# Performance work log

Hardware: AMD Instinct MI355X
Metric: run time of the kernel (lower is better)

## Reference

```python
import jax, jax.numpy as jnp
import numpy as np

N_NODES = 50000
N_EDGES = 800000
K_HOPS = 4
F_IN, F_HID, A_DIM = 6, 128, 3


def gcn_norm(edge_index, edge_weight, num_nodes):
    # TAGConv(normalize=True) uses gcn_norm WITHOUT added self-loops:
    # norm = D^{-1/2}[src] * w * D^{-1/2}[dst], deg computed at target (col).
    row, col = edge_index[0], edge_index[1]
    deg = jax.ops.segment_sum(edge_weight, col, num_segments=num_nodes)
    deg_inv_sqrt = jnp.where(deg > 0, jax.lax.rsqrt(deg), 0.0)
    return deg_inv_sqrt[row] * edge_weight * deg_inv_sqrt[col]


def tag_conv(x, edge_index, norm_w, W, b):
    # out = sum_{k=0..K} (A_hat^k x) @ W[k] + b ; W: [K+1, in, out]
    row, col = edge_index[0], edge_index[1]
    out = x @ W[0]
    xk = x
    for k in range(1, W.shape[0]):
        # one sparse propagation hop: gather at src, scale, scatter-add at dst
        xk = jax.ops.segment_sum(norm_w[:, None] * xk[row], col, num_segments=x.shape[0])
        out = out + xk @ W[k]
    return out + b


def setup_inputs() -> dict:
    key = jax.random.key(0)
    ks = jax.random.split(key, 5)
    x = jax.random.normal(ks[0], (N_NODES, F_IN), dtype=jnp.float32)
    edge_index = jax.random.randint(ks[1], (2, N_EDGES), 0, N_NODES, dtype=jnp.int32)
    edge_weight = jax.random.uniform(ks[2], (N_EDGES,), dtype=jnp.float32)
    s1 = float(1.0 / np.sqrt(F_IN))
    s2 = float(1.0 / np.sqrt(F_HID))
    W1 = jax.random.uniform(ks[3], (K_HOPS + 1, F_IN, F_HID), minval=-s1, maxval=s1, dtype=jnp.float32)
    b1 = jnp.zeros((F_HID,), jnp.float32)
    W2 = jax.random.uniform(ks[4], (K_HOPS + 1, F_HID, 2 * A_DIM), minval=-s2, maxval=s2, dtype=jnp.float32)
    b2 = jnp.zeros((2 * A_DIM,), jnp.float32)
    return {"x": x, "edge_index": edge_index, "edge_weight": edge_weight,
            "W1": W1, "b1": b1, "W2": W2, "b2": b2}


def reference(x, edge_index, edge_weight, W1, b1, W2, b2):
    norm_w = gcn_norm(edge_index, edge_weight, x.shape[0])
    h = jax.nn.relu(tag_conv(x, edge_index, norm_w, W1, b1))
    out = tag_conv(h, edge_index, norm_w, W2, b2)
    mu = jnp.tanh(out[..., :A_DIM])
    logvar = jnp.tanh(out[..., A_DIM:])
    sigma = jnp.exp(2.0 * logvar)
    return mu, sigma
```

## Files before the change

### kernel.cpp

```cpp
#include <hip/hip_runtime.h>

#define NN 50000
#define NE 800000
#define KH 4
#define FIN 6
#define FH 128
#define FO 6
#define ADIM 3
#define NN6 (NN * 6)
#define NN8 (NN * 8)
#define NBKT 196
#define EPB 2048
#define NPB 391
#define CAP 6144
#define ROWMASK 0xFFFFFu
#define NEPAD (NE + NBKT * 1024)

typedef unsigned int u32;
typedef _Float16 f16;
typedef f16 f16x8 __attribute__((ext_vector_type(8)));

struct __align__(8) Edge { u32 r; float w; };

__device__ __forceinline__ float h2f_bits(u32 hb) {
    union { unsigned short us; f16 h; } c; c.us = (unsigned short)hb; return (float)c.h;
}
__device__ __forceinline__ u32 f2h_bits(float f) {
    union { unsigned short us; f16 h; } c; c.h = (f16)f; return (u32)c.us;
}
__device__ __forceinline__ u32 pack2(float a, float b) {
    return f2h_bits(a) | (f2h_bits(b) << 16);
}

__global__ void bucket_hist(const int* __restrict__ col, u32* __restrict__ ghist) {
    __shared__ u32 h[NBKT];
    for (int t = threadIdx.x; t < NBKT; t += 256) h[t] = 0;
    __syncthreads();
    int base = blockIdx.x * EPB;
#pragma unroll
    for (int i = 0; i < EPB / 256; ++i) {
        int e = base + i * 256 + threadIdx.x;
        if (e < NE) atomicAdd(&h[((u32)col[e]) >> 8], 1u);
    }
    __syncthreads();
    for (int t = threadIdx.x; t < NBKT; t += 256)
        if (h[t]) atomicAdd(&ghist[t], h[t]);
}

__global__ void bucket_scan(const u32* __restrict__ ghist, u32* __restrict__ bbase,
                            u32* __restrict__ bcur,
                            const float* __restrict__ W1, const float* __restrict__ W2,
                            float* __restrict__ W1T, float* __restrict__ W2T) {
    __shared__ u32 sh[256];
    int t = threadIdx.x;
    u32 v = (t < NBKT) ? ghist[t] : 0;
    sh[t] = v;
    __syncthreads();
    for (int off = 1; off < 256; off <<= 1) {
        u32 u = (t >= off) ? sh[t - off] : 0;
        __syncthreads();
        sh[t] += u;
        __syncthreads();
    }
    if (t < NBKT) { bbase[t] = sh[t] - v; bcur[t] = sh[t] - v; }
    if (t == NBKT - 1) bbase[NBKT] = sh[t];
    for (int idx = t; idx < 30 * FH; idx += 256) {
        int f = idx / 30, i = idx - f * 30;
        W1T[idx] = W1[i * FH + f];
        int k = i / 6, a = i - k * 6;
        W2T[idx] = W2[((size_t)k * FH + f) * FO + a];
    }
}

__global__ __launch_bounds__(256) void partition_kernel(
        const int* __restrict__ row, const int* __restrict__ col,
        const float* __restrict__ w, u32* __restrict__ bcur,
        Edge* __restrict__ etmp) {
    __shared__ u32 hcnt[NBKT];
    __shared__ u32 hloc[NBKT];
    __shared__ u32 hglb[NBKT];
    __shared__ u32 smeta[EPB];
    __shared__ float swt[EPB];
    __shared__ u32 sgid[EPB];
    __shared__ u32 sc[256];
    for (int t = threadIdx.x; t < NBKT; t += 256) hcnt[t] = 0;
    __syncthreads();
    int base = blockIdx.x * EPB;
    u32 m_[8]; float w_[8]; u32 b_[8]; u32 rk_[8]; int v_[8];
#pragma unroll
    for (int i = 0; i < 8; ++i) {
        int e = base + i * 256 + threadIdx.x;
        v_[i] = e < NE;
        if (v_[i]) {
            u32 c = (u32)col[e];
            u32 r = (u32)row[e];
            b_[i] = c >> 8;
            m_[i] = ((c & 255u) << 20) | r;
            w_[i] = w[e];
            rk_[i] = atomicAdd(&hcnt[b_[i]], 1u);
        }
    }
    __syncthreads();
    {
        int t = threadIdx.x;
        u32 v = (t < NBKT) ? hcnt[t] : 0;
        sc[t] = v;
        __syncthreads();
        for (int off = 1; off < 256; off <<= 1) {
            u32 u = (t >= off) ? sc[t - off] : 0;
            __syncthreads();
            sc[t] += u;
            __syncthreads();
        }
        if (t < NBKT) hloc[t] = sc[t] - v;
    }
    __syncthreads();
    for (int t = threadIdx.x; t < NBKT; t += 256)
        if (hcnt[t]) hglb[t] = atomicAdd(&bcur[t], hcnt[t]);
    __syncthreads();
#pragma unroll
    for (int i = 0; i < 8; ++i) if (v_[i]) {
        u32 slot = hloc[b_[i]] + rk_[i];
        smeta[slot] = m_[i];
        swt[slot] = w_[i];
        sgid[slot] = hglb[b_[i]] + rk_[i];
    }
    __syncthreads();
    int tot = NE - base; if (tot > EPB) tot = EPB;
    for (int s = threadIdx.x; s < tot; s += 256) {
        Edge ed; ed.r = smeta[s]; ed.w = swt[s];
        etmp[sgid[s]] = ed;
    }
}

__global__ __launch_bounds__(256) void bucket_csr(
        const u32* __restrict__ bbase, const Edge* __restrict__ etmp,
        u32* __restrict__ edges, int* __restrict__ offs, int* __restrict__ eoff,
        float* __restrict__ dinv) {
    int b = blockIdx.x;
    int t = threadIdx.x;
    u32 s = bbase[b], e = bbase[b + 1];
    int cnt = (int)(e - s);
    u32 rb = s + (u32)b * 1024u;
    int node0 = b << 8;
    int nloc = NN - node0; if (nloc > 256) nloc = 256;
    __shared__ u32 ncnt[256];
    __shared__ float nsum[256];
    __shared__ u32 ncur[256];
    __shared__ u32 sc[256];
    __shared__ u32 stage[CAP];
    ncnt[t] = 0; nsum[t] = 0.f;
    __syncthreads();
    for (int i = t; i < cnt; i += 256) {
        Edge ed = etmp[s + i];
        u32 cl = ed.r >> 20;
        atomicAdd(&ncnt[cl], 1u);
        atomicAdd(&nsum[cl], ed.w);
    }
    __syncthreads();
    u32 v = ncnt[t];
    u32 pv = (v + 3u) & ~3u;
    sc[t] = pv;
    __syncthreads();
    for (int off = 1; off < 256; off <<= 1) {
        u32 u = (t >= off) ? sc[t - off] : 0;
        __syncthreads();
        sc[t] += u;
        __syncthreads();
    }
    u32 excl = sc[t] - pv;
    u32 ptot = sc[255];
    ncur[t] = excl;
    if (t < nloc) {
        offs[node0 + t] = (int)(rb + excl);
        eoff[node0 + t] = (int)(rb + excl + pv);
        float d = nsum[t];
        dinv[node0 + t] = d > 0.f ? rsqrtf(d) : 0.f;
    }
    __syncthreads();
    for (int i = t; i < cnt; i += 256) {
        Edge ed = etmp[s + i];
        u32 cl = ed.r >> 20;
        u32 slot = atomicAdd(&ncur[cl], 1u);
        u32 pw = (ed.r & ROWMASK) | (f2h_bits(ed.w) << 16);
        if (slot < CAP) stage[slot] = pw;
        else edges[rb + slot] = pw;
    }
    if (t < nloc) {
        for (u32 slot = excl + v; slot < excl + pv; ++slot) {
            if (slot < CAP) stage[slot] = 0u;
            else edges[rb + slot] = 0u;
        }
    }
    __syncthreads();
    int lim = (int)(ptot < CAP ? ptot : CAP);
    for (int i = t; i < lim; i += 256) edges[rb + i] = stage[i];
}

__global__ void pad_x(const float* __restrict__ x, f16* __restrict__ xpad) {
    int t = blockIdx.x * blockDim.x + threadIdx.x;
    if (t >= NN8) return;
    int n = t >> 3, c = t & 7;
    xpad[t] = (c < 6) ? (f16)x[n * 6 + c] : (f16)0.f;
}

__device__ __forceinline__ void gath(const f16* __restrict__ xp, u32 r, float w,
                                     float& a0, float& a1, float& a2,
                                     float& a3, float& a4, float& a5) {
    f16x8 v = *(const f16x8*)(xp + (size_t)r * 8);
    a0 += w * (float)v[0]; a1 += w * (float)v[1]; a2 += w * (float)v[2];
    a3 += w * (float)v[3]; a4 += w * (float)v[4]; a5 += w * (float)v[5];
}

#define HOP_HEAD \
    int t = blockIdx.x * blockDim.x + threadIdx.x; \
    int n = t >> 2, j = t & 3; \
    if (n >= NN) return; \
    int s = offs[n], e = eoff[n]; \
    float a0 = 0.f, a1 = 0.f, a2 = 0.f, a3 = 0.f, a4 = 0.f, a5 = 0.f;

#define HOP_REDUCE \
    _Pragma("unroll") \
    for (int d = 1; d < 4; d <<= 1) { \
        a0 += __shfl_xor(a0, d); a1 += __shfl_xor(a1, d); a2 += __shfl_xor(a2, d); \
        a3 += __shfl_xor(a3, d); a4 += __shfl_xor(a4, d); a5 += __shfl_xor(a5, d); \
    }

__global__ void hop4(const int* __restrict__ offs, const int* __restrict__ eoff,
                     const u32* __restrict__ edges,
                     const f16* __restrict__ xprev, const float* __restrict__ yadd,
                     f16* __restrict__ xnext) {
    HOP_HEAD
    for (int i = s + 4 * j; i < e; i += 16) {
        int4 q = *(const int4*)(edges + i);
        { u32 wd = (u32)q.x; gath(xprev, wd & 0xFFFFu, h2f_bits(wd >> 16), a0, a1, a2, a3, a4, a5); }
        { u32 wd = (u32)q.y; gath(xprev, wd & 0xFFFFu, h2f_bits(wd >> 16), a0, a1, a2, a3, a4, a5); }
        { u32 wd = (u32)q.z; gath(xprev, wd & 0xFFFFu, h2f_bits(wd >> 16), a0, a1, a2, a3, a4, a5); }
        { u32 wd = (u32)q.w; gath(xprev, wd & 0xFFFFu, h2f_bits(wd >> 16), a0, a1, a2, a3, a4, a5); }
    }
    HOP_REDUCE
    float v0 = j == 0 ? a0 : j == 1 ? a2 : j == 2 ? a4 : 0.f;
    float v1 = j == 0 ? a1 : j == 1 ? a3 : j == 2 ? a5 : 0.f;
    if (yadd && j < 3) {
        v0 += yadd[(size_t)n * 32 + 2 * j];
        v1 += yadd[(size_t)n * 32 + 2 * j + 1];
    }
    ((u32*)xnext)[(size_t)n * 4 + j] = pack2(v0, v1);
}

__global__ void hop4_norm(const int* __restrict__ offs, const int* __restrict__ eoff,
                          u32* __restrict__ edges,
                          const float* __restrict__ dinv, const f16* __restrict__ xpad,
                          f16* __restrict__ xnext) {
    HOP_HEAD
    float dn = dinv[n];
    for (int i = s + 4 * j; i < e; i += 16) {
        int4 q = *(const int4*)(edges + i);
        int4 nq;
        {
            u32 wd = (u32)q.x; u32 r = wd & 0xFFFFu;
            float wn = h2f_bits(wd >> 16) * dn * dinv[r];
            nq.x = (int)(r | (f2h_bits(wn) << 16));
            gath(xpad, r, wn, a0, a1, a2, a3, a4, a5);
        }
        {
            u32 wd = (u32)q.y; u32 r = wd & 0xFFFFu;
            float wn = h2f_bits(wd >> 16) * dn * dinv[r];
            nq.y = (int)(r | (f2h_bits(wn) << 16));
            gath(xpad, r, wn, a0, a1, a2, a3, a4, a5);
        }
        {
            u32 wd = (u32)q.z; u32 r = wd & 0xFFFFu;
            float wn = h2f_bits(wd >> 16) * dn * dinv[r];
            nq.z = (int)(r | (f2h_bits(wn) << 16));
            gath(xpad, r, wn, a0, a1, a2, a3, a4, a5);
        }
        {
            u32 wd = (u32)q.w; u32 r = wd & 0xFFFFu;
            float wn = h2f_bits(wd >> 16) * dn * dinv[r];
            nq.w = (int)(r | (f2h_bits(wn) << 16));
            gath(xpad, r, wn, a0, a1, a2, a3, a4, a5);
        }
        *(int4*)(edges + i) = nq;
    }
    HOP_REDUCE
    float v0 = j == 0 ? a0 : j == 1 ? a2 : j == 2 ? a4 : 0.f;
    float v1 = j == 0 ? a1 : j == 1 ? a3 : j == 2 ? a5 : 0.f;
    ((u32*)xnext)[(size_t)n * 4 + j] = pack2(v0, v1);
}

__global__ void hop4_final(const int* __restrict__ offs, const int* __restrict__ eoff,
                           const u32* __restrict__ edges,
                           const f16* __restrict__ xprev, const float* __restrict__ y0,
                           float* __restrict__ out) {
    HOP_HEAD
    for (int i = s + 4 * j; i < e; i += 16) {
        int4 q = *(const int4*)(edges + i);
        { u32 wd = (u32)q.x; gath(xprev, wd & 0xFFFFu, h2f_bits(wd >> 16), a0, a1, a2, a3, a4, a5); }
        { u32 wd = (u32)q.y; gath(xprev, wd & 0xFFFFu, h2f_bits(wd >> 16), a0, a1, a2, a3, a4, a5); }
        { u32 wd = (u32)q.z; gath(xprev, wd & 0xFFFFu, h2f_bits(wd >> 16), a0, a1, a2, a3, a4, a5); }
        { u32 wd = (u32)q.w; gath(xprev, wd & 0xFFFFu, h2f_bits(wd >> 16), a0, a1, a2, a3, a4, a5); }
    }
    HOP_REDUCE
    if (j < 3) {
        float mv = (j == 0 ? a0 : j == 1 ? a1 : a2) + y0[(size_t)n * 32 + j];
        float sv = (j == 0 ? a3 : j == 1 ? a4 : a5) + y0[(size_t)n * 32 + 3 + j];
        out[n * ADIM + j] = tanhf(mv);
        out[NN * ADIM + n * ADIM + j] = expf(2.f * tanhf(sv));
    }
}

__global__ __launch_bounds__(256) void fused_dense_kernel(
        const float* __restrict__ x, const f16* __restrict__ xs,
        const float* __restrict__ W1T, const float* __restrict__ b1,
        const float* __restrict__ W2T, const float* __restrict__ b2,
        float* __restrict__ ys, f16* __restrict__ y4h) {
    int n = blockIdx.x * 256 + threadIdx.x;
    if (n >= NN) return;
    float in[30];
    {
        const float* xr = x + (size_t)n * 6;
        float2 v0 = *(const float2*)xr;
        float2 v1 = *(const float2*)(xr + 2);
        float2 v2 = *(const float2*)(xr + 4);
        in[0] = v0.x; in[1] = v0.y; in[2] = v1.x;
        in[3] = v1.y; in[4] = v2.x; in[5] = v2.y;
    }
#pragma unroll
    for (int k = 0; k < 4; ++k) {
        f16x8 v = *(const f16x8*)(xs + (size_t)k * NN8 + (size_t)n * 8);
#pragma unroll
        for (int c = 0; c < 6; ++c) in[6 + k * 6 + c] = (float)v[c];
    }
    float acc[30];
#pragma unroll
    for (int o = 0; o < 30; ++o) acc[o] = (o < 6) ? b2[o] : 0.f;
#pragma unroll 2
    for (int f = 0; f < FH; ++f) {
        const float* w1c = W1T + f * 30;
        float h = b1[f];
#pragma unroll
        for (int i = 0; i < 30; ++i) h = fmaf(in[i], w1c[i], h);
        h = h > 0.f ? h : 0.f;
        const float* w2c = W2T + f * 30;
#pragma unroll
        for (int o = 0; o < 30; ++o) acc[o] = fmaf(h, w2c[o], acc[o]);
    }
    float* yr = ys + (size_t)n * 32;
#pragma unroll
    for (int o4 = 0; o4 < 6; ++o4)
        *(float4*)(yr + o4 * 4) = make_float4(acc[o4 * 4], acc[o4 * 4 + 1],
                                              acc[o4 * 4 + 2], acc[o4 * 4 + 3]);
    u32* yh = (u32*)(y4h + (size_t)n * 8);
    yh[0] = pack2(acc[24], acc[25]);
    yh[1] = pack2(acc[26], acc[27]);
    yh[2] = pack2(acc[28], acc[29]);
}

extern "C" void kernel_launch(void* const* d_in, const int* in_sizes, int n_in,
                              void* d_out, int out_size, void* d_ws, size_t ws_size,
                              hipStream_t stream) {
    const float* x  = (const float*)d_in[0];
    const int*   ei = (const int*)d_in[1];
    const float* ew = (const float*)d_in[2];
    const float* W1 = (const float*)d_in[3];
    const float* b1 = (const float*)d_in[4];
    const float* W2 = (const float*)d_in[5];
    const float* b2 = (const float*)d_in[6];
    float* out = (float*)d_out;

    const int* row = ei;
    const int* col = ei + NE;

    f16*   xpad  = (f16*)d_ws;
    f16*   xs    = xpad + NN8;
    f16*   y4h   = xs + (size_t)KH * NN8;
    f16*   za    = y4h + NN8;
    f16*   zb    = za + NN8;
    float* ys    = (float*)(zb + NN8);
    float* W1T   = ys + (size_t)NN * 32;
    float* W2T   = W1T + 30 * FH;
    Edge*  etmp  = (Edge*)(W2T + 30 * FH);
    u32*   edges = (u32*)(etmp + NE);
    u32*   ghist = edges + NEPAD;
    u32*   bbase = ghist + NBKT;
    u32*   bcur  = bbase + NBKT + 1;
    int*   offs  = (int*)(bcur + NBKT);
    int*   eoff  = offs + NN;
    float* dinv  = (float*)(eoff + NN);

    const int B = 256;
    const int gHop = (NN * 4 + B - 1) / B;
    const int gPad = (NN8 + B - 1) / B;
    const int gFD  = (NN + B - 1) / B;

    hipMemsetAsync(ghist, 0, NBKT * sizeof(u32), stream);
    bucket_hist<<<NPB, B, 0, stream>>>(col, ghist);
    bucket_scan<<<1, B, 0, stream>>>(ghist, bbase, bcur, W1, W2, W1T, W2T);
    partition_kernel<<<NPB, B, 0, stream>>>(row, col, ew, bcur, etmp);
    bucket_csr<<<NBKT, B, 0, stream>>>(bbase, etmp, edges, offs, eoff, dinv);
    pad_x<<<gPad, B, 0, stream>>>(x, xpad);

    hop4_norm<<<gHop, B, 0, stream>>>(offs, eoff, edges, dinv, xpad, xs);
    for (int k = 2; k <= KH; ++k)
        hop4<<<gHop, B, 0, stream>>>(offs, eoff, edges,
                                     xs + (size_t)(k - 2) * NN8, nullptr,
                                     xs + (size_t)(k - 1) * NN8);

    fused_dense_kernel<<<gFD, B, 0, stream>>>(x, xs, W1T, b1, W2T, b2, ys, y4h);

    hop4<<<gHop, B, 0, stream>>>(offs, eoff, edges, y4h, ys + 18, za);
    hop4<<<gHop, B, 0, stream>>>(offs, eoff, edges, za, ys + 12, zb);
    hop4<<<gHop, B, 0, stream>>>(offs, eoff, edges, zb, ys + 6, za);
    hop4_final<<<gHop, B, 0, stream>>>(offs, eoff, edges, za, ys, out);
}
```

Measured before the change: 163.8 us.

## Split fused dense kernel across hidden-feature chunks with separate reduction pass

The fused dense MLP kernel, which had only 196 blocks of one thread per node, is split into 4 chunks over the 128 hidden features. Each chunk writes partial 32-float accumulators to a workspace buffer, and a new reduce kernel sums them, adds the bias and writes ys and y4h. This raises parallelism on a device with many CUs, at the cost of an extra launch and about 25 MB of partial-sum traffic. The weight transpose also moves from the single-block scan kernel into the pad_x kernel so that it runs across many threads.

```diff
diff --git a/kernel.cpp b/kernel.cpp
--- a/kernel.cpp
+++ b/kernel.cpp
@@ -15,6 +15,8 @@
 #define CAP 6144
 #define ROWMASK 0xFFFFFu
 #define NEPAD (NE + NBKT * 1024)
+#define NCH 4
+#define NDB 196
 
 typedef unsigned int u32;
 typedef _Float16 f16;
@@ -48,9 +50,7 @@
 }
 
 __global__ void bucket_scan(const u32* __restrict__ ghist, u32* __restrict__ bbase,
-                            u32* __restrict__ bcur,
-                            const float* __restrict__ W1, const float* __restrict__ W2,
-                            float* __restrict__ W1T, float* __restrict__ W2T) {
+                            u32* __restrict__ bcur) {
     __shared__ u32 sh[256];
     int t = threadIdx.x;
     u32 v = (t < NBKT) ? ghist[t] : 0;
@@ -64,12 +64,6 @@
     }
     if (t < NBKT) { bbase[t] = sh[t] - v; bcur[t] = sh[t] - v; }
     if (t == NBKT - 1) bbase[NBKT] = sh[t];
-    for (int idx = t; idx < 30 * FH; idx += 256) {
-        int f = idx / 30, i = idx - f * 30;
-        W1T[idx] = W1[i * FH + f];
-        int k = i / 6, a = i - k * 6;
-        W2T[idx] = W2[((size_t)k * FH + f) * FO + a];
-    }
 }
 
 __global__ __launch_bounds__(256) void partition_kernel(
@@ -197,8 +191,16 @@
     for (int i = t; i < lim; i += 256) edges[rb + i] = stage[i];
 }
 
-__global__ void pad_x(const float* __restrict__ x, f16* __restrict__ xpad) {
+__global__ void pad_x(const float* __restrict__ x, f16* __restrict__ xpad,
+                      const float* __restrict__ W1, const float* __restrict__ W2,
+                      float* __restrict__ W1T, float* __restrict__ W2T) {
     int t = blockIdx.x * blockDim.x + threadIdx.x;
+    if (t < 30 * FH) {
+        int f = t / 30, i = t - f * 30;
+        W1T[t] = W1[i * FH + f];
+        int k = i / 6, a = i - k * 6;
+        W2T[t] = W2[((size_t)k * FH + f) * FO + a];
+    }
     if (t >= NN8) return;
     int n = t >> 3, c = t & 7;
     xpad[t] = (c < 6) ? (f16)x[n * 6 + c] : (f16)0.f;
@@ -313,9 +315,11 @@
 __global__ __launch_bounds__(256) void fused_dense_kernel(
         const float* __restrict__ x, const f16* __restrict__ xs,
         const float* __restrict__ W1T, const float* __restrict__ b1,
-        const float* __restrict__ W2T, const float* __restrict__ b2,
-        float* __restrict__ ys, f16* __restrict__ y4h) {
-    int n = blockIdx.x * 256 + threadIdx.x;
+        const float* __restrict__ W2T,
+        float* __restrict__ pacc) {
+    int bb = blockIdx.x;
+    int c = bb & (NCH - 1);
+    int n = (bb >> 2) * 256 + threadIdx.x;
     if (n >= NN) return;
     float in[30];
     {
@@ -330,13 +334,15 @@
     for (int k = 0; k < 4; ++k) {
         f16x8 v = *(const f16x8*)(xs + (size_t)k * NN8 + (size_t)n * 8);
 #pragma unroll
-        for (int c = 0; c < 6; ++c) in[6 + k * 6 + c] = (float)v[c];
-    }
-    float acc[30];
-#pragma unroll
-    for (int o = 0; o < 30; ++o) acc[o] = (o < 6) ? b2[o] : 0.f;
+        for (int cc = 0; cc < 6; ++cc) in[6 + k * 6 + cc] = (float)v[cc];
+    }
+    float acc[32];
+#pragma unroll
+    for (int o = 0; o < 32; ++o) acc[o] = 0.f;
+    int f0 = c * (FH / NCH);
 #pragma unroll 2
-    for (int f = 0; f < FH; ++f) {
+    for (int fi = 0; fi < FH / NCH; ++fi) {
+        int f = f0 + fi;
         const float* w1c = W1T + f * 30;
         float h = b1[f];
 #pragma unroll
@@ -346,6 +352,32 @@
 #pragma unroll
         for (int o = 0; o < 30; ++o) acc[o] = fmaf(h, w2c[o], acc[o]);
     }
+    float* pr = pacc + ((size_t)c * NN + n) * 32;
+#pragma unroll
+    for (int o4 = 0; o4 < 8; ++o4)
+        *(float4*)(pr + o4 * 4) = make_float4(acc[o4 * 4], acc[o4 * 4 + 1],
+                                              acc[o4 * 4 + 2], acc[o4 * 4 + 3]);
+}
+
+__global__ void reduce_dense(const float* __restrict__ pacc, const float* __restrict__ b2,
+                             float* __restrict__ ys, f16* __restrict__ y4h) {
+    int n = blockIdx.x * 256 + threadIdx.x;
+    if (n >= NN) return;
+    float acc[32];
+#pragma unroll
+    for (int o = 0; o < 32; ++o) acc[o] = 0.f;
+#pragma unroll
+    for (int c = 0; c < NCH; ++c) {
+        const float* pr = pacc + ((size_t)c * NN + n) * 32;
+#pragma unroll
+        for (int o4 = 0; o4 < 8; ++o4) {
+            float4 v = *(const float4*)(pr + o4 * 4);
+            acc[o4 * 4 + 0] += v.x; acc[o4 * 4 + 1] += v.y;
+            acc[o4 * 4 + 2] += v.z; acc[o4 * 4 + 3] += v.w;
+        }
+    }
+#pragma unroll
+    for (int o = 0; o < 6; ++o) acc[o] += b2[o];
     float* yr = ys + (size_t)n * 32;
 #pragma unroll
     for (int o4 = 0; o4 < 6; ++o4)
@@ -378,7 +410,8 @@
     f16*   za    = y4h + NN8;
     f16*   zb    = za + NN8;
     float* ys    = (float*)(zb + NN8);
-    float* W1T   = ys + (size_t)NN * 32;
+    float* pacc  = ys + (size_t)NN * 32;
+    float* W1T   = pacc + (size_t)NCH * NN * 32;
     float* W2T   = W1T + 30 * FH;
     Edge*  etmp  = (Edge*)(W2T + 30 * FH);
     u32*   edges = (u32*)(etmp + NE);
@@ -392,14 +425,13 @@
     const int B = 256;
     const int gHop = (NN * 4 + B - 1) / B;
     const int gPad = (NN8 + B - 1) / B;
-    const int gFD  = (NN + B - 1) / B;
 
     hipMemsetAsync(ghist, 0, NBKT * sizeof(u32), stream);
     bucket_hist<<<NPB, B, 0, stream>>>(col, ghist);
-    bucket_scan<<<1, B, 0, stream>>>(ghist, bbase, bcur, W1, W2, W1T, W2T);
+    bucket_scan<<<1, B, 0, stream>>>(ghist, bbase, bcur);
     partition_kernel<<<NPB, B, 0, stream>>>(row, col, ew, bcur, etmp);
     bucket_csr<<<NBKT, B, 0, stream>>>(bbase, etmp, edges, offs, eoff, dinv);
-    pad_x<<<gPad, B, 0, stream>>>(x, xpad);
+    pad_x<<<gPad, B, 0, stream>>>(x, xpad, W1, W2, W1T, W2T);
 
     hop4_norm<<<gHop, B, 0, stream>>>(offs, eoff, edges, dinv, xpad, xs);
     for (int k = 2; k <= KH; ++k)
@@ -407,7 +439,8 @@
                                      xs + (size_t)(k - 2) * NN8, nullptr,
                                      xs + (size_t)(k - 1) * NN8);
 
-    fused_dense_kernel<<<gFD, B, 0, stream>>>(x, xs, W1T, b1, W2T, b2, ys, y4h);
+    fused_dense_kernel<<<NDB * NCH, B, 0, stream>>>(x, xs, W1T, b1, W2T, pacc);
+    reduce_dense<<<NDB, B, 0, stream>>>(pacc, b2, ys, y4h);
 
     hop4<<<gHop, B, 0, stream>>>(offs, eoff, edges, y4h, ys + 18, za);
     hop4<<<gHop, B, 0, stream>>>(offs, eoff, edges, za, ys + 12, zb);
```

Result: faster. 148.5 us (-9.4%).

## Split dense hidden dimension across four threads per node with LDS reduction

Applied to the files above, without the earlier changes.

The fused dense kernel used one thread per node and looped over all 128 hidden features, giving only about 196 blocks. It now assigns four threads per node, each handling a quarter of the hidden features, and sums their partial 30-wide outputs through shared memory across 782 blocks. This raises parallelism in the dense stage at the cost of a 33 KB LDS buffer and a block barrier, which may limit occupancy. Separately, the ghist memset and the weight transposes move into pad_x, which now runs first, removing a memset call and taking work off the single-block scan.

```diff
diff --git a/kernel.cpp b/kernel.cpp
--- a/kernel.cpp
+++ b/kernel.cpp
@@ -7,7 +7,6 @@
 #define FH 128
 #define FO 6
 #define ADIM 3
-#define NN6 (NN * 6)
 #define NN8 (NN * 8)
 #define NBKT 196
 #define EPB 2048
@@ -15,6 +14,7 @@
 #define CAP 6144
 #define ROWMASK 0xFFFFFu
 #define NEPAD (NE + NBKT * 1024)
+#define DRB 782
 
 typedef unsigned int u32;
 typedef _Float16 f16;
@@ -48,9 +48,7 @@
 }
 
 __global__ void bucket_scan(const u32* __restrict__ ghist, u32* __restrict__ bbase,
-                            u32* __restrict__ bcur,
-                            const float* __restrict__ W1, const float* __restrict__ W2,
-                            float* __restrict__ W1T, float* __restrict__ W2T) {
+                            u32* __restrict__ bcur) {
     __shared__ u32 sh[256];
     int t = threadIdx.x;
     u32 v = (t < NBKT) ? ghist[t] : 0;
@@ -64,12 +62,6 @@
     }
     if (t < NBKT) { bbase[t] = sh[t] - v; bcur[t] = sh[t] - v; }
     if (t == NBKT - 1) bbase[NBKT] = sh[t];
-    for (int idx = t; idx < 30 * FH; idx += 256) {
-        int f = idx / 30, i = idx - f * 30;
-        W1T[idx] = W1[i * FH + f];
-        int k = i / 6, a = i - k * 6;
-        W2T[idx] = W2[((size_t)k * FH + f) * FO + a];
-    }
 }
 
 __global__ __launch_bounds__(256) void partition_kernel(
@@ -197,8 +189,18 @@
     for (int i = t; i < lim; i += 256) edges[rb + i] = stage[i];
 }
 
-__global__ void pad_x(const float* __restrict__ x, f16* __restrict__ xpad) {
+__global__ void pad_x(const float* __restrict__ x, f16* __restrict__ xpad,
+                      const float* __restrict__ W1, const float* __restrict__ W2,
+                      float* __restrict__ W1T, float* __restrict__ W2T,
+                      u32* __restrict__ ghist) {
     int t = blockIdx.x * blockDim.x + threadIdx.x;
+    if (t < NBKT) ghist[t] = 0;
+    if (t < 30 * FH) {
+        int f = t / 30, i = t - f * 30;
+        W1T[t] = W1[i * FH + f];
+        int k = i / 6, a = i - k * 6;
+        W2T[t] = W2[((size_t)k * FH + f) * FO + a];
+    }
     if (t >= NN8) return;
     int n = t >> 3, c = t & 7;
     xpad[t] = (c < 6) ? (f16)x[n * 6 + c] : (f16)0.f;
@@ -257,30 +259,14 @@
     for (int i = s + 4 * j; i < e; i += 16) {
         int4 q = *(const int4*)(edges + i);
         int4 nq;
-        {
-            u32 wd = (u32)q.x; u32 r = wd & 0xFFFFu;
-            float wn = h2f_bits(wd >> 16) * dn * dinv[r];
-            nq.x = (int)(r | (f2h_bits(wn) << 16));
-            gath(xpad, r, wn, a0, a1, a2, a3, a4, a5);
-        }
-        {
-            u32 wd = (u32)q.y; u32 r = wd & 0xFFFFu;
-            float wn = h2f_bits(wd >> 16) * dn * dinv[r];
-            nq.y = (int)(r | (f2h_bits(wn) << 16));
-            gath(xpad, r, wn, a0, a1, a2, a3, a4, a5);
-        }
-        {
-            u32 wd = (u32)q.z; u32 r = wd & 0xFFFFu;
-            float wn = h2f_bits(wd >> 16) * dn * dinv[r];
-            nq.z = (int)(r | (f2h_bits(wn) << 16));
-            gath(xpad, r, wn, a0, a1, a2, a3, a4, a5);
-        }
-        {
-            u32 wd = (u32)q.w; u32 r = wd & 0xFFFFu;
-            float wn = h2f_bits(wd >> 16) * dn * dinv[r];
-            nq.w = (int)(r | (f2h_bits(wn) << 16));
-            gath(xpad, r, wn, a0, a1, a2, a3, a4, a5);
-        }
+        { u32 wd = (u32)q.x; u32 r = wd & 0xFFFFu; float wn = h2f_bits(wd >> 16) * dn * dinv[r];
+          nq.x = (int)(r | (f2h_bits(wn) << 16)); gath(xpad, r, wn, a0, a1, a2, a3, a4, a5); }
+        { u32 wd = (u32)q.y; u32 r = wd & 0xFFFFu; float wn = h2f_bits(wd >> 16) * dn * dinv[r];
+          nq.y = (int)(r | (f2h_bits(wn) << 16)); gath(xpad, r, wn, a0, a1, a2, a3, a4, a5); }
+        { u32 wd = (u32)q.z; u32 r = wd & 0xFFFFu; float wn = h2f_bits(wd >> 16) * dn * dinv[r];
+          nq.z = (int)(r | (f2h_bits(wn) << 16)); gath(xpad, r, wn, a0, a1, a2, a3, a4, a5); }
+        { u32 wd = (u32)q.w; u32 r = wd & 0xFFFFu; float wn = h2f_bits(wd >> 16) * dn * dinv[r];
+          nq.w = (int)(r | (f2h_bits(wn) << 16)); gath(xpad, r, wn, a0, a1, a2, a3, a4, a5); }
         *(int4*)(edges + i) = nq;
     }
     HOP_REDUCE
@@ -310,51 +296,77 @@
     }
 }
 
-__global__ __launch_bounds__(256) void fused_dense_kernel(
+__global__ __launch_bounds__(256) void dense_reduce_kernel(
         const float* __restrict__ x, const f16* __restrict__ xs,
         const float* __restrict__ W1T, const float* __restrict__ b1,
         const float* __restrict__ W2T, const float* __restrict__ b2,
         float* __restrict__ ys, f16* __restrict__ y4h) {
-    int n = blockIdx.x * 256 + threadIdx.x;
-    if (n >= NN) return;
-    float in[30];
-    {
-        const float* xr = x + (size_t)n * 6;
-        float2 v0 = *(const float2*)xr;
-        float2 v1 = *(const float2*)(xr + 2);
-        float2 v2 = *(const float2*)(xr + 4);
-        in[0] = v0.x; in[1] = v0.y; in[2] = v1.x;
-        in[3] = v1.y; in[4] = v2.x; in[5] = v2.y;
-    }
-#pragma unroll
-    for (int k = 0; k < 4; ++k) {
-        f16x8 v = *(const f16x8*)(xs + (size_t)k * NN8 + (size_t)n * 8);
-#pragma unroll
-        for (int c = 0; c < 6; ++c) in[6 + k * 6 + c] = (float)v[c];
-    }
+    __shared__ float red[256 * 33];
+    int t = threadIdx.x;
+    int c = t >> 6, nl = t & 63;
+    int n = blockIdx.x * 64 + nl;
     float acc[30];
 #pragma unroll
-    for (int o = 0; o < 30; ++o) acc[o] = (o < 6) ? b2[o] : 0.f;
+    for (int o = 0; o < 30; ++o) acc[o] = 0.f;
+    if (n < NN) {
+        float in[30];
+        {
+            const float* xr = x + (size_t)n * 6;
+            float2 v0 = *(const float2*)xr;
+            float2 v1 = *(const float2*)(xr + 2);
+            float2 v2 = *(const float2*)(xr + 4);
+            in[0] = v0.x; in[1] = v0.y; in[2] = v1.x;
+            in[3] = v1.y; in[4] = v2.x; in[5] = v2.y;
+        }
+#pragma unroll
+        for (int k = 0; k < 4; ++k) {
+            f16x8 v = *(const f16x8*)(xs + (size_t)k * NN8 + (size_t)n * 8);
+#pragma unroll
+            for (int cc = 0; cc < 6; ++cc) in[6 + k * 6 + cc] = (float)v[cc];
+        }
+        int f0 = c * (FH / 4);
 #pragma unroll 2
-    for (int f = 0; f < FH; ++f) {
-        const float* w1c = W1T + f * 30;
-        float h = b1[f];
-#pragma unroll
-        for (int i = 0; i < 30; ++i) h = fmaf(in[i], w1c[i], h);
-        h = h > 0.f ? h : 0.f;
-        const float* w2c = W2T + f * 30;
-#pragma unroll
-        for (int o = 0; o < 30; ++o) acc[o] = fmaf(h, w2c[o], acc[o]);
-    }
-    float* yr = ys + (size_t)n * 32;
-#pragma unroll
-    for (int o4 = 0; o4 < 6; ++o4)
-        *(float4*)(yr + o4 * 4) = make_float4(acc[o4 * 4], acc[o4 * 4 + 1],
-                                              acc[o4 * 4 + 2], acc[o4 * 4 + 3]);
-    u32* yh = (u32*)(y4h + (size_t)n * 8);
-    yh[0] = pack2(acc[24], acc[25]);
-    yh[1] = pack2(acc[26], acc[27]);
-    yh[2] = pack2(acc[28], acc[29]);
+        for (int fi = 0; fi < FH / 4; ++fi) {
+            int f = f0 + fi;
+            const float* w1c = W1T + f * 30;
+            float h = b1[f];
+#pragma unroll
+            for (int i = 0; i < 30; ++i) h = fmaf(in[i], w1c[i], h);
+            h = h > 0.f ? h : 0.f;
+            const float* w2c = W2T + f * 30;
+#pragma unroll
+            for (int o = 0; o < 30; ++o) acc[o] = fmaf(h, w2c[o], acc[o]);
+        }
+    }
+    float* my = &red[t * 33];
+#pragma unroll
+    for (int o = 0; o < 30; ++o) my[o] = acc[o];
+    __syncthreads();
+    int nl2 = t >> 2, q = t & 3;
+    int n2 = blockIdx.x * 64 + nl2;
+    if (n2 >= NN) return;
+    float r[8];
+#pragma unroll
+    for (int i = 0; i < 8; ++i) {
+        int o = q * 8 + i;
+        float s = 0.f;
+        if (o < 30) {
+#pragma unroll
+            for (int cc = 0; cc < 4; ++cc) s += red[(cc * 64 + nl2) * 33 + o];
+            if (o < 6) s += b2[o];
+        }
+        r[i] = s;
+    }
+    if (q < 3) {
+        float* yr = ys + (size_t)n2 * 32 + q * 8;
+        *(float4*)yr = make_float4(r[0], r[1], r[2], r[3]);
+        *(float4*)(yr + 4) = make_float4(r[4], r[5], r[6], r[7]);
+    } else {
+        u32* yh = (u32*)(y4h + (size_t)n2 * 8);
+        yh[0] = pack2(r[0], r[1]);
+        yh[1] = pack2(r[2], r[3]);
+        yh[2] = pack2(r[4], r[5]);
+    }
 }
 
 extern "C" void kernel_launch(void* const* d_in, const int* in_sizes, int n_in,
@@ -392,14 +404,12 @@
     const int B = 256;
     const int gHop = (NN * 4 + B - 1) / B;
     const int gPad = (NN8 + B - 1) / B;
-    const int gFD  = (NN + B - 1) / B;
-
-    hipMemsetAsync(ghist, 0, NBKT * sizeof(u32), stream);
+
+    pad_x<<<gPad, B, 0, stream>>>(x, xpad, W1, W2, W1T, W2T, ghist);
     bucket_hist<<<NPB, B, 0, stream>>>(col, ghist);
-    bucket_scan<<<1, B, 0, stream>>>(ghist, bbase, bcur, W1, W2, W1T, W2T);
+    bucket_scan<<<1, B, 0, stream>>>(ghist, bbase, bcur);
     partition_kernel<<<NPB, B, 0, stream>>>(row, col, ew, bcur, etmp);
     bucket_csr<<<NBKT, B, 0, stream>>>(bbase, etmp, edges, offs, eoff, dinv);
-    pad_x<<<gPad, B, 0, stream>>>(x, xpad);
 
     hop4_norm<<<gHop, B, 0, stream>>>(offs, eoff, edges, dinv, xpad, xs);
     for (int k = 2; k <= KH; ++k)
@@ -407,7 +417,7 @@
                                      xs + (size_t)(k - 2) * NN8, nullptr,
                                      xs + (size_t)(k - 1) * NN8);
 
-    fused_dense_kernel<<<gFD, B, 0, stream>>>(x, xs, W1T, b1, W2T, b2, ys, y4h);
+    dense_reduce_kernel<<<DRB, B, 0, stream>>>(x, xs, W1T, b1, W2T, b2, ys, y4h);
 
     hop4<<<gHop, B, 0, stream>>>(offs, eoff, edges, y4h, ys + 18, za);
     hop4<<<gHop, B, 0, stream>>>(offs, eoff, edges, za, ys + 12, zb);
```

Result: slower. 170.2 us (+3.9%).
